# Kernel optimization log

Measured on AMD Instinct MI355X. Metric: run time of the kernel, lower is better.

Reference implementation:

```python
import jax, jax.numpy as jnp
import numpy as np

ALPHA = 0.0005625
R_TIA = 0.1
DENOM = 2.0 * 1.5 * 0.025  # 2*n*VT = 0.075
V_D = 0.1
BN_EPS = 1e-5
KSZ, STRIDE, PAD = 3, 1, 1


def _unfold(x, k, s, p):
    # torch F.unfold equivalent: (N, C*k*k, L), channel-major then (ki, kj)
    N, C, H, W = x.shape
    Ho = (H + 2 * p - k) // s + 1
    Wo = (W + 2 * p - k) // s + 1
    xp = jnp.pad(x, ((0, 0), (0, 0), (p, p), (p, p)))
    cols = [xp[:, :, i:i + s * Ho:s, j:j + s * Wo:s]
            for i in range(k) for j in range(k)]  # each (N, C, Ho, Wo)
    patches = jnp.stack(cols, axis=2)             # (N, C, k*k, Ho, Wo)
    return patches.reshape(N, C * k * k, Ho * Wo), Ho, Wo


def setup_inputs() -> dict:
    key = jax.random.key(0)
    kx, kt = jax.random.split(key)
    x = jax.random.normal(kx, (32, 3, 32, 32), dtype=jnp.float32)
    theta = jax.random.uniform(kt, (3 * KSZ * KSZ, 64), dtype=jnp.float32,
                               minval=0.0, maxval=9.0)
    gamma = jnp.ones((64,), dtype=jnp.float32)
    beta = jnp.zeros((64,), dtype=jnp.float32)
    return {"x": x, "theta": theta, "gamma": gamma, "beta": beta}


def reference(x, theta, gamma, beta):
    N = x.shape[0]
    C_out = theta.shape[1]
    patches, Ho, Wo = _unfold(x, KSZ, STRIDE, PAD)      # (N, K, L)
    V_j = patches.transpose(0, 2, 1)[..., None]          # (N, L, K, 1)
    t1 = jax.nn.softplus((V_j - theta) / DENOM) ** 2     # (N, L, K, Cout)
    t2 = jax.nn.softplus((V_j - theta - V_D) / DENOM) ** 2
    I_k = ALPHA * jnp.sum(t1 - t2, axis=2)               # (N, L, Cout)
    V_out = (I_k * R_TIA).transpose(0, 2, 1).reshape(N, C_out, Ho, Wo)
    # BatchNorm2d in training mode: biased batch statistics
    mean = V_out.mean(axis=(0, 2, 3), keepdims=True)
    var = V_out.var(axis=(0, 2, 3), keepdims=True)
    V_hat = (V_out - mean) * jax.lax.rsqrt(var + BN_EPS)
    return V_hat * gamma[None, :, None, None] + beta[None, :, None, None]
```

## Files before the change

### kernel.cpp

```cpp
#include <hip/hip_runtime.h>


constexpr float INV_D  = 13.333333333333334f;
constexpr double CD    = 0.26359713811572677;
constexpr float C_NEG  = (float)CD;
constexpr double LN2SQ = 0.4804530139182014;
constexpr double OUT_SC = 5.625e-5 * LN2SQ;
constexpr float TA = (float)((1.0 - CD * CD) / LN2SQ);
constexpr float TB = (float)((1.0 - CD * CD * CD) / LN2SQ);
constexpr float E_THR = 0.125f;
constexpr int   NCHUNK = 512;

__global__ __launch_bounds__(256)
void nlc_exp(const float* __restrict__ x, float* __restrict__ xe)
{
    const int i = blockIdx.x * 256 + threadIdx.x;
    float4 v = reinterpret_cast<const float4*>(x)[i];
    v.x = fminf(__expf(v.x * INV_D), 3.0e38f);
    v.y = fminf(__expf(v.y * INV_D), 3.0e38f);
    v.z = fminf(__expf(v.z * INV_D), 3.0e38f);
    v.w = fminf(__expf(v.w * INV_D), 3.0e38f);
    reinterpret_cast<float4*>(xe)[i] = v;
}

__global__ __launch_bounds__(256)
void nlc_compute(const float* __restrict__ xe, const float* __restrict__ theta,
                 float* __restrict__ vout, float* __restrict__ psum,
                 float* __restrict__ psq)
{
    __shared__ alignas(16) float thc[27 * 16];
    const int tid   = threadIdx.x;
    const int chunk = blockIdx.x >> 2;
    const int cbase = (blockIdx.x & 3) * 16;

    for (int i = tid; i < 27 * 16; i += 256) {
        const int k = i >> 4, cc = i & 15;
        thc[i] = __expf(-theta[k * 64 + cbase + cc] * INV_D);
    }
    __syncthreads();

    const int lane = tid & 63;
    const int wv   = tid >> 6;
    const int p    = chunk * 64 + lane;
    const int n    = p >> 10;
    const int hw   = p & 1023;
    const int h    = hw >> 5;
    const int w    = hw & 31;

    const float* xn = xe + n * 3072;
    const float4* thv4 = reinterpret_cast<const float4*>(thc);

    int ad[9];
    unsigned okm = 0;
#pragma unroll
    for (int ki = 0; ki < 3; ++ki) {
#pragma unroll
        for (int kj = 0; kj < 3; ++kj) {
            const int  hh = h + ki - 1;
            const int  ww = w + kj - 1;
            const bool ok = ((unsigned)hh < 32u) & ((unsigned)ww < 32u);
            ad[ki * 3 + kj] = ok ? (hh * 32 + ww) : 0;
            okm |= (unsigned)ok << (ki * 3 + kj);
        }
    }

    float acc0 = 0.f, acc1 = 0.f, acc2 = 0.f, acc3 = 0.f;

#pragma unroll 1
    for (int ci = 0; ci < 3; ++ci) {
        float Ev[9];
#pragma unroll
        for (int j = 0; j < 9; ++j) {
            const float ev = xn[ci * 1024 + ad[j]];
            Ev[j] = ((okm >> j) & 1u) ? ev : 1.0f;
        }
#pragma unroll
        for (int j = 0; j < 9; ++j) {
            const float4 t4 = thv4[(ci * 9 + j) * 4 + wv];
            const float E0 = Ev[j] * t4.x;
            const float E1 = Ev[j] * t4.y;
            const float E2 = Ev[j] * t4.z;
            const float E3 = Ev[j] * t4.w;

            if (__all(E0 <= E_THR)) {
                acc0 = fmaf(E0 * E0, fmaf(-TB, E0, TA), acc0);
            } else {
                const float l1 = __log2f(1.0f + E0);
                const float l2 = __log2f(fmaf(E0, C_NEG, 1.0f));
                acc0 = fmaf(l1, l1, acc0);
                acc0 = fmaf(-l2, l2, acc0);
            }
            if (__all(E1 <= E_THR)) {
                acc1 = fmaf(E1 * E1, fmaf(-TB, E1, TA), acc1);
            } else {
                const float l1 = __log2f(1.0f + E1);
                const float l2 = __log2f(fmaf(E1, C_NEG, 1.0f));
                acc1 = fmaf(l1, l1, acc1);
                acc1 = fmaf(-l2, l2, acc1);
            }
            if (__all(E2 <= E_THR)) {
                acc2 = fmaf(E2 * E2, fmaf(-TB, E2, TA), acc2);
            } else {
                const float l1 = __log2f(1.0f + E2);
                const float l2 = __log2f(fmaf(E2, C_NEG, 1.0f));
                acc2 = fmaf(l1, l1, acc2);
                acc2 = fmaf(-l2, l2, acc2);
            }
            if (__all(E3 <= E_THR)) {
                acc3 = fmaf(E3 * E3, fmaf(-TB, E3, TA), acc3);
            } else {
                const float l1 = __log2f(1.0f + E3);
                const float l2 = __log2f(fmaf(E3, C_NEG, 1.0f));
                acc3 = fmaf(l1, l1, acc3);
                acc3 = fmaf(-l2, l2, acc3);
            }
        }
    }

    const float acc[4] = {acc0, acc1, acc2, acc3};
#pragma unroll
    for (int i = 0; i < 4; ++i) {
        const int   c  = cbase + wv * 4 + i;
        const float vo = acc[i];
        vout[(n << 16) + (c << 10) + hw] = vo;

        float s = vo, q = vo * vo;
#pragma unroll
        for (int off = 32; off > 0; off >>= 1) {
            s += __shfl_xor(s, off, 64);
            q += __shfl_xor(q, off, 64);
        }
        if (lane == 0) {
            psum[c * NCHUNK + chunk] = s;
            psq [c * NCHUNK + chunk] = q;
        }
    }
}

__global__ __launch_bounds__(256)
void nlc_finish(const float* __restrict__ psum, const float* __restrict__ psq,
                const float* __restrict__ gamma, const float* __restrict__ beta,
                float* __restrict__ vout)
{
    const int b   = blockIdx.x;
    const int c   = b >> 3;
    const int seg = b & 7;
    const int tid = threadIdx.x;

    float4* p0 = reinterpret_cast<float4*>(vout)
               + ((seg * 4 + 0) * 64 + c) * 256 + tid;
    float4* p1 = p0 + 64 * 256;
    float4* p2 = p1 + 64 * 256;
    float4* p3 = p2 + 64 * 256;
    float4 v0 = *p0, v1 = *p1, v2 = *p2, v3 = *p3;

    double s = (double)psum[c * NCHUNK + tid] + (double)psum[c * NCHUNK + 256 + tid];
    double q = (double)psq [c * NCHUNK + tid] + (double)psq [c * NCHUNK + 256 + tid];
#pragma unroll
    for (int off = 32; off > 0; off >>= 1) {
        s += __shfl_xor(s, off, 64);
        q += __shfl_xor(q, off, 64);
    }
    __shared__ double ls[4], lq[4];
    __shared__ float  scsh[2];
    if ((tid & 63) == 0) { ls[tid >> 6] = s; lq[tid >> 6] = q; }
    __syncthreads();
    if (tid == 0) {
        s = ls[0] + ls[1] + ls[2] + ls[3];
        q = lq[0] + lq[1] + lq[2] + lq[3];
        const double inv    = 1.0 / 32768.0;
        const double mean_a = s * inv;
        const double var_a  = q * inv - mean_a * mean_a;
        const double var_V  = var_a * OUT_SC * OUT_SC;
        const double rstd   = 1.0 / sqrt(var_V + 1e-5);
        const double sc     = (double)gamma[c] * rstd * OUT_SC;
        const double sh     = (double)beta[c] - mean_a * sc;
        scsh[0] = (float)sc;
        scsh[1] = (float)sh;
    }
    __syncthreads();
    const float sc = scsh[0];
    const float sh = scsh[1];

#define NLC_BN4(v) \
    v.x = fmaf(v.x, sc, sh); v.y = fmaf(v.y, sc, sh); \
    v.z = fmaf(v.z, sc, sh); v.w = fmaf(v.w, sc, sh);
    NLC_BN4(v0) NLC_BN4(v1) NLC_BN4(v2) NLC_BN4(v3)
#undef NLC_BN4

    *p0 = v0; *p1 = v1; *p2 = v2; *p3 = v3;
}

extern "C" void kernel_launch(void* const* d_in, const int* in_sizes, int n_in,
                              void* d_out, int out_size, void* d_ws, size_t ws_size,
                              hipStream_t stream)
{
    const float* x     = (const float*)d_in[0];
    const float* theta = (const float*)d_in[1];
    const float* gamma = (const float*)d_in[2];
    const float* beta  = (const float*)d_in[3];
    float* out = (float*)d_out;

    float* psum = (float*)d_ws;
    float* psq  = psum + 64 * NCHUNK;
    float* xe   = psq  + 64 * NCHUNK;

    nlc_exp    <<<96, 256, 0, stream>>>(x, xe);
    nlc_compute<<<NCHUNK * 4, 256, 0, stream>>>(xe, theta, out, psum, psq);
    nlc_finish <<<512, 256, 0, stream>>>(psum, psq, gamma, beta, out);
}
```

Before: 33.63 us.

## Process two pixels per thread and drop the small-E polynomial fast path

Each thread now computes two output pixels (rows hw and hw+64) for its four channels, which halves the block count and the number of partial-sum chunks. The theta values loaded from shared memory are reused across both pixels. The wave-uniform branch that swapped in a cubic polynomial when E was small is removed, so every term now always evaluates two log2 calls. This gives more independent work per thread and removes branch divergence checks, but adds transcendental work wherever the polynomial path used to be taken.

After: 37.75 us. 12.3% more time.

```diff
diff --git a/kernel.cpp b/kernel.cpp
--- a/kernel.cpp
+++ b/kernel.cpp
@@ -6,10 +6,7 @@
 constexpr float C_NEG  = (float)CD;
 constexpr double LN2SQ = 0.4804530139182014;
 constexpr double OUT_SC = 5.625e-5 * LN2SQ;
-constexpr float TA = (float)((1.0 - CD * CD) / LN2SQ);
-constexpr float TB = (float)((1.0 - CD * CD * CD) / LN2SQ);
-constexpr float E_THR = 0.125f;
-constexpr int   NCHUNK = 512;
+constexpr int   NSC = 256;
 
 __global__ __launch_bounds__(256)
 void nlc_exp(const float* __restrict__ x, float* __restrict__ xe)
@@ -30,7 +27,7 @@
 {
     __shared__ alignas(16) float thc[27 * 16];
     const int tid   = threadIdx.x;
-    const int chunk = blockIdx.x >> 2;
+    const int sc    = blockIdx.x >> 2;
     const int cbase = (blockIdx.x & 3) * 16;
 
     for (int i = tid; i < 27 * 16; i += 256) {
@@ -41,98 +38,90 @@
 
     const int lane = tid & 63;
     const int wv   = tid >> 6;
-    const int p    = chunk * 64 + lane;
-    const int n    = p >> 10;
-    const int hw   = p & 1023;
-    const int h    = hw >> 5;
-    const int w    = hw & 31;
+    const int p0   = sc * 128 + lane;
+    const int n    = p0 >> 10;
+    const int hw0  = p0 & 1023;
+    const int hw1  = hw0 + 64;
+    const int h0   = hw0 >> 5;
+    const int w    = hw0 & 31;
 
     const float* xn = xe + n * 3072;
     const float4* thv4 = reinterpret_cast<const float4*>(thc);
 
-    int ad[9];
-    unsigned okm = 0;
+    int ad0[9], ad1[9];
+    unsigned okm0 = 0, okm1 = 0;
 #pragma unroll
     for (int ki = 0; ki < 3; ++ki) {
 #pragma unroll
         for (int kj = 0; kj < 3; ++kj) {
-            const int  hh = h + ki - 1;
-            const int  ww = w + kj - 1;
-            const bool ok = ((unsigned)hh < 32u) & ((unsigned)ww < 32u);
-            ad[ki * 3 + kj] = ok ? (hh * 32 + ww) : 0;
-            okm |= (unsigned)ok << (ki * 3 + kj);
-        }
-    }
-
-    float acc0 = 0.f, acc1 = 0.f, acc2 = 0.f, acc3 = 0.f;
+            const int  ww  = w + kj - 1;
+            const bool okw = (unsigned)ww < 32u;
+            const int  hA  = h0 + ki - 1;
+            const int  hB  = hA + 2;
+            const bool okA = ((unsigned)hA < 32u) & okw;
+            const bool okB = ((unsigned)hB < 32u) & okw;
+            const int  jj  = ki * 3 + kj;
+            ad0[jj] = okA ? (hA * 32 + ww) : 0;
+            ad1[jj] = okB ? (hB * 32 + ww) : 0;
+            okm0 |= (unsigned)okA << jj;
+            okm1 |= (unsigned)okB << jj;
+        }
+    }
+
+    float a00 = 0.f, a01 = 0.f, a02 = 0.f, a03 = 0.f;
+    float a10 = 0.f, a11 = 0.f, a12 = 0.f, a13 = 0.f;
 
 #pragma unroll 1
     for (int ci = 0; ci < 3; ++ci) {
-        float Ev[9];
+        float Ev0[9], Ev1[9];
 #pragma unroll
         for (int j = 0; j < 9; ++j) {
-            const float ev = xn[ci * 1024 + ad[j]];
-            Ev[j] = ((okm >> j) & 1u) ? ev : 1.0f;
+            const float e0 = xn[ci * 1024 + ad0[j]];
+            const float e1 = xn[ci * 1024 + ad1[j]];
+            Ev0[j] = ((okm0 >> j) & 1u) ? e0 : 1.0f;
+            Ev1[j] = ((okm1 >> j) & 1u) ? e1 : 1.0f;
         }
 #pragma unroll
         for (int j = 0; j < 9; ++j) {
             const float4 t4 = thv4[(ci * 9 + j) * 4 + wv];
-            const float E0 = Ev[j] * t4.x;
-            const float E1 = Ev[j] * t4.y;
-            const float E2 = Ev[j] * t4.z;
-            const float E3 = Ev[j] * t4.w;
-
-            if (__all(E0 <= E_THR)) {
-                acc0 = fmaf(E0 * E0, fmaf(-TB, E0, TA), acc0);
-            } else {
-                const float l1 = __log2f(1.0f + E0);
-                const float l2 = __log2f(fmaf(E0, C_NEG, 1.0f));
-                acc0 = fmaf(l1, l1, acc0);
-                acc0 = fmaf(-l2, l2, acc0);
-            }
-            if (__all(E1 <= E_THR)) {
-                acc1 = fmaf(E1 * E1, fmaf(-TB, E1, TA), acc1);
-            } else {
-                const float l1 = __log2f(1.0f + E1);
-                const float l2 = __log2f(fmaf(E1, C_NEG, 1.0f));
-                acc1 = fmaf(l1, l1, acc1);
-                acc1 = fmaf(-l2, l2, acc1);
-            }
-            if (__all(E2 <= E_THR)) {
-                acc2 = fmaf(E2 * E2, fmaf(-TB, E2, TA), acc2);
-            } else {
-                const float l1 = __log2f(1.0f + E2);
-                const float l2 = __log2f(fmaf(E2, C_NEG, 1.0f));
-                acc2 = fmaf(l1, l1, acc2);
-                acc2 = fmaf(-l2, l2, acc2);
-            }
-            if (__all(E3 <= E_THR)) {
-                acc3 = fmaf(E3 * E3, fmaf(-TB, E3, TA), acc3);
-            } else {
-                const float l1 = __log2f(1.0f + E3);
-                const float l2 = __log2f(fmaf(E3, C_NEG, 1.0f));
-                acc3 = fmaf(l1, l1, acc3);
-                acc3 = fmaf(-l2, l2, acc3);
-            }
-        }
-    }
-
-    const float acc[4] = {acc0, acc1, acc2, acc3};
+#define NLC_TERM(ACC, EV, TH) {                         \
+            const float E  = (EV) * (TH);               \
+            const float l1 = __log2f(1.0f + E);         \
+            const float l2 = __log2f(fmaf(E, C_NEG, 1.0f)); \
+            ACC = fmaf(l1, l1, ACC);                    \
+            ACC = fmaf(-l2, l2, ACC); }
+            NLC_TERM(a00, Ev0[j], t4.x)
+            NLC_TERM(a01, Ev0[j], t4.y)
+            NLC_TERM(a02, Ev0[j], t4.z)
+            NLC_TERM(a03, Ev0[j], t4.w)
+            NLC_TERM(a10, Ev1[j], t4.x)
+            NLC_TERM(a11, Ev1[j], t4.y)
+            NLC_TERM(a12, Ev1[j], t4.z)
+            NLC_TERM(a13, Ev1[j], t4.w)
+#undef NLC_TERM
+        }
+    }
+
+    const float accA[4] = {a00, a01, a02, a03};
+    const float accB[4] = {a10, a11, a12, a13};
 #pragma unroll
     for (int i = 0; i < 4; ++i) {
         const int   c  = cbase + wv * 4 + i;
-        const float vo = acc[i];
-        vout[(n << 16) + (c << 10) + hw] = vo;
-
-        float s = vo, q = vo * vo;
+        const float v0 = accA[i];
+        const float v1 = accB[i];
+        vout[(n << 16) + (c << 10) + hw0] = v0;
+        vout[(n << 16) + (c << 10) + hw1] = v1;
+
+        float s = v0 + v1;
+        float q = fmaf(v0, v0, v1 * v1);
 #pragma unroll
         for (int off = 32; off > 0; off >>= 1) {
             s += __shfl_xor(s, off, 64);
             q += __shfl_xor(q, off, 64);
         }
         if (lane == 0) {
-            psum[c * NCHUNK + chunk] = s;
-            psq [c * NCHUNK + chunk] = q;
+            psum[c * NSC + sc] = s;
+            psq [c * NSC + sc] = q;
         }
     }
 }
@@ -154,8 +143,8 @@
     float4* p3 = p2 + 64 * 256;
     float4 v0 = *p0, v1 = *p1, v2 = *p2, v3 = *p3;
 
-    double s = (double)psum[c * NCHUNK + tid] + (double)psum[c * NCHUNK + 256 + tid];
-    double q = (double)psq [c * NCHUNK + tid] + (double)psq [c * NCHUNK + 256 + tid];
+    double s = (double)psum[c * NSC + tid];
+    double q = (double)psq [c * NSC + tid];
 #pragma unroll
     for (int off = 32; off > 0; off >>= 1) {
         s += __shfl_xor(s, off, 64);
@@ -202,10 +191,10 @@
     float* out = (float*)d_out;
 
     float* psum = (float*)d_ws;
-    float* psq  = psum + 64 * NCHUNK;
-    float* xe   = psq  + 64 * NCHUNK;
+    float* psq  = psum + 64 * NSC;
+    float* xe   = psq  + 64 * NSC;
 
     nlc_exp    <<<96, 256, 0, stream>>>(x, xe);
-    nlc_compute<<<NCHUNK * 4, 256, 0, stream>>>(xe, theta, out, psum, psq);
+    nlc_compute<<<1024, 256, 0, stream>>>(xe, theta, out, psum, psq);
     nlc_finish <<<512, 256, 0, stream>>>(psum, psq, gamma, beta, out);
 }
```
